# Optimization experiments

Measured on AMD Instinct MI355X. Metric: run time of the kernel, lower is better.

The kernel has to match this reference:

```python
import jax, jax.numpy as jnp
import numpy as np

NEG_SLOPE = 0.2
EPS = 1e-16


def gat_conv(x, edge_index, W, att_src, att_dst, bias, heads, out_ch, concat):
    """PyG-style GATConv (eval mode, add_self_loops=True)."""
    N = x.shape[0]
    h = (x @ W).reshape(N, heads, out_ch)              # [N,H,C]
    loop = jnp.arange(N, dtype=edge_index.dtype)
    src = jnp.concatenate([edge_index[0], loop])       # [E+N]
    dst = jnp.concatenate([edge_index[1], loop])
    a_src = jnp.sum(h * att_src, axis=-1)              # [N,H]
    a_dst = jnp.sum(h * att_dst, axis=-1)
    e = jax.nn.leaky_relu(a_src[src] + a_dst[dst], NEG_SLOPE)  # [E+N,H]
    # segment softmax over destination nodes
    m = jax.ops.segment_max(e, dst, num_segments=N)
    e = jnp.exp(e - m[dst])
    s = jax.ops.segment_sum(e, dst, num_segments=N)
    alpha = e / (s[dst] + EPS)                         # [E+N,H]
    msg = h[src] * alpha[..., None]                    # [E+N,H,C]
    out = jax.ops.segment_sum(msg, dst, num_segments=N)  # [N,H,C]
    out = out.reshape(N, heads * out_ch) if concat else out.mean(axis=1)
    return out + bias


def setup_inputs() -> dict:
    key = jax.random.key(0)
    ks = jax.random.split(key, 11)
    N, F, E = 100000, 128, 1600000
    H1, C1 = 4, 16
    H2, C2 = 1, 16
    return {
        "x": jax.random.normal(ks[0], (N, F), dtype=jnp.float32),
        "edge_index": jax.random.randint(ks[1], (2, E), 0, N, dtype=jnp.int64) if jax.config.jax_enable_x64 else jax.random.randint(ks[1], (2, E), 0, N).astype(jnp.int32),
        "W1": jax.random.normal(ks[2], (F, H1 * C1), dtype=jnp.float32) * 0.1,
        "att_src1": jax.random.normal(ks[3], (H1, C1), dtype=jnp.float32) * 0.1,
        "att_dst1": jax.random.normal(ks[4], (H1, C1), dtype=jnp.float32) * 0.1,
        "bias1": jax.random.normal(ks[5], (H1 * C1,), dtype=jnp.float32) * 0.1,
        "W2": jax.random.normal(ks[6], (H1 * C1, H2 * C2), dtype=jnp.float32) * 0.1,
        "att_src2": jax.random.normal(ks[7], (H2, C2), dtype=jnp.float32) * 0.1,
        "att_dst2": jax.random.normal(ks[8], (H2, C2), dtype=jnp.float32) * 0.1,
        "bias2": jax.random.normal(ks[9], (C2,), dtype=jnp.float32) * 0.1,
    }


def reference(x, edge_index, W1, att_src1, att_dst1, bias1, W2, att_src2, att_dst2, bias2):
    # dropout is identity in eval mode
    h = gat_conv(x, edge_index, W1, att_src1, att_dst1, bias1, heads=4, out_ch=16, concat=True)
    h = jax.nn.elu(h)
    h = gat_conv(h, edge_index, W2, att_src2, att_dst2, bias2, heads=1, out_ch=16, concat=False)
    return jax.nn.log_softmax(h, axis=1)
```

## Files before the change

### kernel.cpp

```cpp
#include <hip/hip_runtime.h>
#include <hip/hip_fp16.h>
#include <hip/hip_bf16.h>
#include <math.h>


#define LRELU(v) ((v) > 0.f ? (v) : 0.2f * (v))
#define CAP 128
#define BSH 8
#define BCAP 5120
#define CHK 2048

typedef __attribute__((ext_vector_type(8))) short short8;
typedef __attribute__((ext_vector_type(4))) float float4v;

static __device__ __forceinline__ short f2bf(float f) {
    __hip_bfloat16 b = __float2bfloat16(f);
    return *reinterpret_cast<short*>(&b);
}

__global__ __launch_bounds__(256) void k_scatter(const int* __restrict__ ei, int* __restrict__ cursor,
                                                 int* __restrict__ stage, int E, int NBK) {
    __shared__ int sval[CHK];
    __shared__ int gaddr[CHK];
    __shared__ int sdst[CHK];
    __shared__ int hist[512];
    __shared__ int lbase[512];
    __shared__ int cnt2[512];
    __shared__ int gdelta[512];
    __shared__ int sA[512];
    int tid = threadIdx.x;
    int e0 = blockIdx.x * CHK;
    int nedge = E - e0; if (nedge > CHK) nedge = CHK;

    for (int i = tid; i < 512; i += 256) { hist[i] = 0; cnt2[i] = 0; }
    __syncthreads();
    for (int j = tid; j < nedge; j += 256) {
        int d = ei[E + e0 + j];
        sdst[j] = d;
        atomicAdd(&hist[d >> BSH], 1);
    }
    __syncthreads();
    sA[tid] = hist[tid]; sA[tid + 256] = hist[tid + 256];
    __syncthreads();
    for (int off = 1; off < 512; off <<= 1) {
        int r0 = sA[tid] + ((tid >= off) ? sA[tid - off] : 0);
        int r1 = sA[tid + 256] + ((tid + 256 >= off) ? sA[tid + 256 - off] : 0);
        __syncthreads();
        sA[tid] = r0; sA[tid + 256] = r1;
        __syncthreads();
    }
    for (int i = tid; i < 512; i += 256) lbase[i] = sA[i] - hist[i];
    __syncthreads();
    for (int b = tid; b < NBK; b += 256) {
        int c = hist[b];
        if (c > 0) {
            int rel = atomicAdd(&cursor[b], c);
            gdelta[b] = b * BCAP + rel - lbase[b];
        }
    }
    __syncthreads();
    for (int j = tid; j < nedge; j += 256) {
        int s = ei[e0 + j];
        int d = sdst[j];
        int b = d >> BSH;
        int r = atomicAdd(&cnt2[b], 1);
        int slot = lbase[b] + r;
        sval[slot]  = s | ((d & ((1 << BSH) - 1)) << 17);
        gaddr[slot] = gdelta[b] + slot;
    }
    __syncthreads();
    for (int s = tid; s < nedge; s += 256) stage[gaddr[s]] = sval[s];
}

__global__ __launch_bounds__(256) void k_bucket_scan(const int* __restrict__ cursor,
                                                     int* __restrict__ gbase,
                                                     int* __restrict__ row_start,
                                                     int NBK, int E, int N) {
    __shared__ int sA[512];
    __shared__ int cnt[512];
    int tid = threadIdx.x;
    for (int i = tid; i < 512; i += 256)
        cnt[i] = (i < NBK) ? cursor[i] : 0;
    __syncthreads();
    sA[tid] = cnt[tid]; sA[tid + 256] = cnt[tid + 256];
    __syncthreads();
    for (int off = 1; off < 512; off <<= 1) {
        int r0 = sA[tid] + ((tid >= off) ? sA[tid - off] : 0);
        int r1 = sA[tid + 256] + ((tid + 256 >= off) ? sA[tid + 256 - off] : 0);
        __syncthreads();
        sA[tid] = r0; sA[tid + 256] = r1;
        __syncthreads();
    }
    for (int i = tid; i < 512; i += 256)
        if (i < NBK) gbase[i] = sA[i] - cnt[i];
    if (tid == 0) { gbase[NBK] = E; row_start[N] = E + N; }
}

__global__ __launch_bounds__(256) void k_build(const int* __restrict__ stage,
                                               const int* __restrict__ gbase,
                                               int* __restrict__ row_start,
                                               int* __restrict__ csr, int N) {
    __shared__ int cnt[256];
    __shared__ int lb[256];
    __shared__ int cur[256];
    __shared__ int sA[256];
    int b = blockIdx.x, tid = threadIdx.x;
    int nodes0 = b << BSH;
    int nnodes = N - nodes0; if (nnodes > 256) nnodes = 256;
    int ebase = gbase[b];
    int ecnt = gbase[b + 1] - ebase;
    const int* sbk = stage + b * BCAP;
    cnt[tid] = (tid < nnodes) ? 1 : 0;
    __syncthreads();
    for (int e = tid; e < ecnt; e += 256) {
        int l = (sbk[e] >> 17) & 255;
        atomicAdd(&cnt[l], 1);
    }
    __syncthreads();
    int myc = cnt[tid];
    sA[tid] = myc;
    __syncthreads();
    for (int off = 1; off < 256; off <<= 1) {
        int r = sA[tid] + ((tid >= off) ? sA[tid - off] : 0);
        __syncthreads();
        sA[tid] = r;
        __syncthreads();
    }
    int gb = ebase + nodes0;
    lb[tid] = sA[tid] - myc;
    cur[tid] = 1;
    __syncthreads();
    if (tid < nnodes) {
        row_start[nodes0 + tid] = gb + lb[tid];
        csr[gb + lb[tid]] = nodes0 + tid;
    }
    __syncthreads();
    for (int e = tid; e < ecnt; e += 256) {
        int v = sbk[e];
        int l = (v >> 17) & 255;
        int src = v & 0x1FFFF;
        int r = atomicAdd(&cur[l], 1);
        csr[gb + lb[l] + r] = src;
    }
}

__global__ __launch_bounds__(128) void k_watt(const float* __restrict__ W1,
                                              const float* __restrict__ att_src,
                                              const float* __restrict__ att_dst,
                                              float* __restrict__ Wc) {
    int k = threadIdx.x;
    #pragma unroll
    for (int h = 0; h < 4; h++) {
        float s = 0.f, d = 0.f;
        #pragma unroll
        for (int c = 0; c < 16; c++) {
            float w = W1[k * 64 + h * 16 + c];
            s += w * att_src[h * 16 + c];
            d += w * att_dst[h * 16 + c];
        }
        Wc[h * 128 + k] = s;
        Wc[(4 + h) * 128 + k] = d;
    }
    #pragma unroll
    for (int col = 8; col < 16; col++) Wc[col * 128 + k] = 0.f;
}

__global__ __launch_bounds__(256) void k_gemm1(const float* __restrict__ x,
                                               const float* __restrict__ W1,
                                               const float* __restrict__ Wc,
                                               __half* __restrict__ h1, float* __restrict__ a_src,
                                               float* __restrict__ a_dst, int N) {
    __shared__ short wt[80 * 136];
    int tid = threadIdx.x;
    for (int i = tid; i < 128 * 64; i += 256) {
        int k = i >> 6, c = i & 63;
        wt[c * 136 + k] = f2bf(W1[i]);
    }
    for (int i = tid; i < 16 * 128; i += 256) {
        int col = i >> 7, k = i & 127;
        wt[(64 + col) * 136 + k] = f2bf(Wc[i]);
    }
    __syncthreads();
    int wave = tid >> 6, lane = tid & 63;
    int m = lane & 15, q = lane >> 4;
    int nbase = blockIdx.x * 64 + wave * 16;
    int anode = nbase + m;
    bool rowok = anode < N;
    const float* xrow = x + (size_t)(rowok ? anode : 0) * 128 + q * 8;

    float4v acc[5];
    #pragma unroll
    for (int ct = 0; ct < 5; ct++)
        #pragma unroll
        for (int r = 0; r < 4; r++) acc[ct][r] = 0.f;

    #pragma unroll
    for (int kc = 0; kc < 4; kc++) {
        float4 u0 = make_float4(0.f, 0.f, 0.f, 0.f), u1 = u0;
        if (rowok) {
            u0 = *(const float4*)(xrow + kc * 32);
            u1 = *(const float4*)(xrow + kc * 32 + 4);
        }
        short8 af;
        af[0] = f2bf(u0.x); af[1] = f2bf(u0.y); af[2] = f2bf(u0.z); af[3] = f2bf(u0.w);
        af[4] = f2bf(u1.x); af[5] = f2bf(u1.y); af[6] = f2bf(u1.z); af[7] = f2bf(u1.w);
        #pragma unroll
        for (int ct = 0; ct < 5; ct++) {
            short8 bf = *(const short8*)&wt[(ct * 16 + m) * 136 + kc * 32 + q * 8];
            acc[ct] = __builtin_amdgcn_mfma_f32_16x16x32_bf16(af, bf, acc[ct], 0, 0, 0);
        }
    }
    #pragma unroll
    for (int ct = 0; ct < 4; ct++) {
        #pragma unroll
        for (int r = 0; r < 4; r++) {
            int n = nbase + q * 4 + r;
            if (n < N) h1[(size_t)n * 64 + ct * 16 + m] = __float2half(acc[ct][r]);
        }
    }
    #pragma unroll
    for (int r = 0; r < 4; r++) {
        int n = nbase + q * 4 + r;
        if (n < N) {
            float v = acc[4][r];
            if (m < 4) a_src[n * 4 + m] = v;
            else if (m < 8) a_dst[n * 4 + (m - 4)] = v;
        }
    }
}

__global__ __launch_bounds__(256) void k_agg1(const int* __restrict__ row_start,
                                              const int* __restrict__ csr_src,
                                              const float* __restrict__ a_src,
                                              const float* __restrict__ a_dst,
                                              const __half* __restrict__ h1,
                                              const float* __restrict__ bias,
                                              float* __restrict__ out1, int N) {
    __shared__ int   sidx[4][CAP];
    __shared__ float sval[4][CAP * 4];
    int wave = threadIdx.x >> 6, lane = threadIdx.x & 63;
    int node = blockIdx.x * 4 + wave;
    if (node >= N) return;
    int row = row_start[node];
    int deg = row_start[node + 1] - row;
    float4 ad = ((const float4*)a_dst)[node];
    float s0 = 0.f, s1 = 0.f, s2 = 0.f, s3 = 0.f;
    for (int j = lane; j < deg; j += 64) {
        int s = csr_src[row + j];
        float4 as = ((const float4*)a_src)[s];
        float e0 = __expf(LRELU(as.x + ad.x));
        float e1 = __expf(LRELU(as.y + ad.y));
        float e2 = __expf(LRELU(as.z + ad.z));
        float e3 = __expf(LRELU(as.w + ad.w));
        if (j < CAP) {
            sidx[wave][j] = s;
            *(float4*)&sval[wave][j * 4] = make_float4(e0, e1, e2, e3);
        }
        s0 += e0; s1 += e1; s2 += e2; s3 += e3;
    }
    #pragma unroll
    for (int m = 1; m < 64; m <<= 1) {
        s0 += __shfl_xor(s0, m, 64);
        s1 += __shfl_xor(s1, m, 64);
        s2 += __shfl_xor(s2, m, 64);
        s3 += __shfl_xor(s3, m, 64);
    }
    int myh = lane >> 4;
    float ssv = myh == 0 ? s0 : myh == 1 ? s1 : myh == 2 ? s2 : s3;
    float adm = myh == 0 ? ad.x : myh == 1 ? ad.y : myh == 2 ? ad.z : ad.w;
    float iv = 1.f / (ssv + 1e-16f);
    float acc = 0.f, accB = 0.f;
    int dc = deg < CAP ? deg : CAP;
    int j = 0;
    for (; j + 8 <= dc; j += 8) {
        int t0 = sidx[wave][j + 0], t1 = sidx[wave][j + 1];
        int t2 = sidx[wave][j + 2], t3 = sidx[wave][j + 3];
        int t4 = sidx[wave][j + 4], t5 = sidx[wave][j + 5];
        int t6 = sidx[wave][j + 6], t7 = sidx[wave][j + 7];
        float e0 = sval[wave][(j + 0) * 4 + myh], e1 = sval[wave][(j + 1) * 4 + myh];
        float e2 = sval[wave][(j + 2) * 4 + myh], e3 = sval[wave][(j + 3) * 4 + myh];
        float e4 = sval[wave][(j + 4) * 4 + myh], e5 = sval[wave][(j + 5) * 4 + myh];
        float e6 = sval[wave][(j + 6) * 4 + myh], e7 = sval[wave][(j + 7) * 4 + myh];
        float g0 = __half2float(h1[(size_t)t0 * 64 + lane]);
        float g1 = __half2float(h1[(size_t)t1 * 64 + lane]);
        float g2 = __half2float(h1[(size_t)t2 * 64 + lane]);
        float g3 = __half2float(h1[(size_t)t3 * 64 + lane]);
        float g4 = __half2float(h1[(size_t)t4 * 64 + lane]);
        float g5 = __half2float(h1[(size_t)t5 * 64 + lane]);
        float g6 = __half2float(h1[(size_t)t6 * 64 + lane]);
        float g7 = __half2float(h1[(size_t)t7 * 64 + lane]);
        acc  += e0 * g0 + e2 * g2 + e4 * g4 + e6 * g6;
        accB += e1 * g1 + e3 * g3 + e5 * g5 + e7 * g7;
    }
    for (; j + 4 <= dc; j += 4) {
        int t0 = sidx[wave][j + 0], t1 = sidx[wave][j + 1];
        int t2 = sidx[wave][j + 2], t3 = sidx[wave][j + 3];
        float e0 = sval[wave][(j + 0) * 4 + myh], e1 = sval[wave][(j + 1) * 4 + myh];
        float e2 = sval[wave][(j + 2) * 4 + myh], e3 = sval[wave][(j + 3) * 4 + myh];
        float g0 = __half2float(h1[(size_t)t0 * 64 + lane]);
        float g1 = __half2float(h1[(size_t)t1 * 64 + lane]);
        float g2 = __half2float(h1[(size_t)t2 * 64 + lane]);
        float g3 = __half2float(h1[(size_t)t3 * 64 + lane]);
        acc  += e0 * g0 + e2 * g2;
        accB += e1 * g1 + e3 * g3;
    }
    for (; j < dc; j++)
        acc += sval[wave][j * 4 + myh] * __half2float(h1[(size_t)sidx[wave][j] * 64 + lane]);
    for (; j < deg; j++) {
        int s = csr_src[row + j];
        float e = __expf(LRELU(a_src[s * 4 + myh] + adm));
        acc += e * __half2float(h1[(size_t)s * 64 + lane]);
    }
    acc = (acc + accB) * iv;
    float o = acc + bias[lane];
    o = (o > 0.f) ? o : (__expf(o) - 1.f);
    out1[(size_t)node * 64 + lane] = o;
}

__global__ __launch_bounds__(256) void k_gemm2(const float* __restrict__ out1,
                                               const float* __restrict__ W2,
                                               const float* __restrict__ att_src,
                                               const float* __restrict__ att_dst,
                                               float* __restrict__ h2, float* __restrict__ a_src,
                                               float* __restrict__ a_dst, int N) {
    __shared__ float ws[64 * 16];
    __shared__ float xs[16 * 65];
    int tid = threadIdx.x;
    for (int i = tid; i < 64 * 16; i += 256) ws[i] = W2[i];
    int n0 = blockIdx.x * 16;
    for (int i = tid; i < 16 * 64; i += 256) {
        int r = i >> 6, c = i & 63;
        int n = n0 + r;
        xs[r * 65 + c] = (n < N) ? out1[(size_t)n * 64 + c] : 0.f;
    }
    __syncthreads();
    int nl = tid >> 4, c = tid & 15;
    int n = n0 + nl;
    float acc = 0.f;
    #pragma unroll
    for (int k = 0; k < 64; k++) acc += xs[nl * 65 + k] * ws[k * 16 + c];
    float asv = acc * att_src[c];
    float adv = acc * att_dst[c];
    #pragma unroll
    for (int m = 1; m < 16; m <<= 1) {
        asv += __shfl_xor(asv, m, 64);
        adv += __shfl_xor(adv, m, 64);
    }
    if (n < N) {
        h2[(size_t)n * 16 + c] = acc;
        if (c == 0) { a_src[n] = asv; a_dst[n] = adv; }
    }
}

#define CAP2 64
__global__ __launch_bounds__(256) void k_agg2(const int* __restrict__ row_start,
                                              const int* __restrict__ csr_src,
                                              const float* __restrict__ a_src,
                                              const float* __restrict__ a_dst,
                                              const float* __restrict__ h2,
                                              const float* __restrict__ bias,
                                              float* __restrict__ out, int N) {
    __shared__ int   sidx[4][2][CAP2];
    __shared__ float sval[4][2][CAP2];
    int wave = threadIdx.x >> 6, lane = threadIdx.x & 63;
    int half = lane >> 5, l32 = lane & 31;
    int node = blockIdx.x * 8 + wave * 2 + half;
    if (node >= N) return;
    int row = row_start[node];
    int deg = row_start[node + 1] - row;
    float ad = a_dst[node];
    float sh = 0.f;
    for (int j = l32; j < deg; j += 32) {
        int s = csr_src[row + j];
        float e = __expf(LRELU(a_src[s] + ad));
        if (j < CAP2) { sidx[wave][half][j] = s; sval[wave][half][j] = e; }
        sh += e;
    }
    #pragma unroll
    for (int m = 1; m < 32; m <<= 1) sh += __shfl_xor(sh, m, 64);
    float iv = 1.f / (sh + 1e-16f);
    int c = l32 & 15, sub = l32 >> 4;
    float acc = 0.f, acc2 = 0.f;
    int dc = deg < CAP2 ? deg : CAP2;
    int j = sub;
    for (; j + 2 < dc; j += 4) {
        int t0 = sidx[wave][half][j], t1 = sidx[wave][half][j + 2];
        float e0 = sval[wave][half][j], e1 = sval[wave][half][j + 2];
        float g0 = h2[(size_t)t0 * 16 + c], g1 = h2[(size_t)t1 * 16 + c];
        acc += e0 * g0; acc2 += e1 * g1;
    }
    for (; j < deg; j += 2) {
        int s; float e;
        if (j < dc) { s = sidx[wave][half][j]; e = sval[wave][half][j]; }
        else { s = csr_src[row + j]; e = __expf(LRELU(a_src[s] + ad)); }
        acc += e * h2[(size_t)s * 16 + c];
    }
    acc += acc2;
    acc += __shfl_xor(acc, 16, 64);
    float val = acc * iv + bias[c];
    float mx = val;
    #pragma unroll
    for (int m = 1; m < 16; m <<= 1) mx = fmaxf(mx, __shfl_xor(mx, m, 64));
    float se = __expf(val - mx);
    #pragma unroll
    for (int m = 1; m < 16; m <<= 1) se += __shfl_xor(se, m, 64);
    float o = val - mx - __logf(se);
    if (sub == 0) out[(size_t)node * 16 + c] = o;
}

extern "C" void kernel_launch(void* const* d_in, const int* in_sizes, int n_in,
                              void* d_out, int out_size, void* d_ws, size_t ws_size,
                              hipStream_t stream) {
    const float* x        = (const float*)d_in[0];
    const int*   ei       = (const int*)d_in[1];
    const float* W1       = (const float*)d_in[2];
    const float* att_src1 = (const float*)d_in[3];
    const float* att_dst1 = (const float*)d_in[4];
    const float* bias1    = (const float*)d_in[5];
    const float* W2       = (const float*)d_in[6];
    const float* att_src2 = (const float*)d_in[7];
    const float* att_dst2 = (const float*)d_in[8];
    const float* bias2    = (const float*)d_in[9];
    float* out = (float*)d_out;

    const int N = in_sizes[0] / 128;
    const int E = in_sizes[1] / 2;
    const int NBK = (N + 255) >> BSH;

    char* p = (char*)d_ws;
    auto alloc = [&](size_t bytes) -> void* {
        void* r = (void*)p;
        p += (bytes + 255) & ~(size_t)255;
        return r;
    };
    __half* h1     = (__half*)alloc((size_t)N * 64 * 2);
    float* out1    = (float*)alloc((size_t)N * 64 * 4);
    float* h2      = (float*)alloc((size_t)N * 16 * 4);
    float* a_src1  = (float*)alloc((size_t)N * 4 * 4);
    float* a_dst1  = (float*)alloc((size_t)N * 4 * 4);
    float* a_src2  = (float*)alloc((size_t)N * 4);
    float* a_dst2  = (float*)alloc((size_t)N * 4);
    float* Wc      = (float*)alloc(16 * 128 * 4);
    int*   row_st  = (int*)alloc((size_t)(N + 1) * 4);
    int*   csr     = (int*)alloc((size_t)(E + N) * 4);
    int*   stage   = (int*)alloc((size_t)NBK * BCAP * 4);
    int*   cursor  = (int*)alloc((size_t)NBK * 4);
    int*   gbase   = (int*)alloc((size_t)(NBK + 1) * 4);
    (void)ws_size; (void)n_in; (void)out_size;

    hipMemsetAsync(cursor, 0, (size_t)NBK * 4, stream);
    k_watt<<<1, 128, 0, stream>>>(W1, att_src1, att_dst1, Wc);
    k_scatter<<<(E + CHK - 1) / CHK, 256, 0, stream>>>(ei, cursor, stage, E, NBK);
    k_bucket_scan<<<1, 256, 0, stream>>>(cursor, gbase, row_st, NBK, E, N);
    k_build<<<NBK, 256, 0, stream>>>(stage, gbase, row_st, csr, N);
    k_gemm1<<<(N + 63) / 64, 256, 0, stream>>>(x, W1, Wc, h1, a_src1, a_dst1, N);
    k_agg1<<<(N + 3) / 4, 256, 0, stream>>>(row_st, csr, a_src1, a_dst1, h1, bias1, out1, N);
    k_gemm2<<<(N + 15) / 16, 256, 0, stream>>>(out1, W2, att_src2, att_dst2, h2, a_src2, a_dst2, N);
    k_agg2<<<(N + 7) / 8, 256, 0, stream>>>(row_st, csr, a_src2, a_dst2, h2, bias2, out, N);
}
```

Baseline: 282.0 us.

## Pack two nodes per wave in layer-1 aggregation and store h2 as fp16

```diff
diff --git a/kernel.cpp b/kernel.cpp
--- a/kernel.cpp
+++ b/kernel.cpp
@@ -5,10 +5,11 @@
 
 
 #define LRELU(v) ((v) > 0.f ? (v) : 0.2f * (v))
-#define CAP 128
 #define BSH 8
 #define BCAP 5120
 #define CHK 2048
+#define CAP1 64
+#define CAP2 64
 
 typedef __attribute__((ext_vector_type(8))) short short8;
 typedef __attribute__((ext_vector_type(4))) float float4v;
@@ -236,92 +237,91 @@
                                               const __half* __restrict__ h1,
                                               const float* __restrict__ bias,
                                               float* __restrict__ out1, int N) {
-    __shared__ int   sidx[4][CAP];
-    __shared__ float sval[4][CAP * 4];
+    __shared__ int   sidx[4][2][CAP1];
+    __shared__ float sval[4][2][CAP1 * 4];
     int wave = threadIdx.x >> 6, lane = threadIdx.x & 63;
-    int node = blockIdx.x * 4 + wave;
+    int half = lane >> 5, l32 = lane & 31;
+    int node = blockIdx.x * 8 + wave * 2 + half;
     if (node >= N) return;
     int row = row_start[node];
     int deg = row_start[node + 1] - row;
     float4 ad = ((const float4*)a_dst)[node];
     float s0 = 0.f, s1 = 0.f, s2 = 0.f, s3 = 0.f;
-    for (int j = lane; j < deg; j += 64) {
+    for (int j = l32; j < deg; j += 32) {
         int s = csr_src[row + j];
         float4 as = ((const float4*)a_src)[s];
         float e0 = __expf(LRELU(as.x + ad.x));
         float e1 = __expf(LRELU(as.y + ad.y));
         float e2 = __expf(LRELU(as.z + ad.z));
         float e3 = __expf(LRELU(as.w + ad.w));
-        if (j < CAP) {
-            sidx[wave][j] = s;
-            *(float4*)&sval[wave][j * 4] = make_float4(e0, e1, e2, e3);
+        if (j < CAP1) {
+            sidx[wave][half][j] = s;
+            *(float4*)&sval[wave][half][j * 4] = make_float4(e0, e1, e2, e3);
         }
         s0 += e0; s1 += e1; s2 += e2; s3 += e3;
     }
     #pragma unroll
-    for (int m = 1; m < 64; m <<= 1) {
+    for (int m = 1; m < 32; m <<= 1) {
         s0 += __shfl_xor(s0, m, 64);
         s1 += __shfl_xor(s1, m, 64);
         s2 += __shfl_xor(s2, m, 64);
         s3 += __shfl_xor(s3, m, 64);
     }
-    int myh = lane >> 4;
+    int myh = l32 >> 3;
     float ssv = myh == 0 ? s0 : myh == 1 ? s1 : myh == 2 ? s2 : s3;
     float adm = myh == 0 ? ad.x : myh == 1 ? ad.y : myh == 2 ? ad.z : ad.w;
     float iv = 1.f / (ssv + 1e-16f);
-    float acc = 0.f, accB = 0.f;
-    int dc = deg < CAP ? deg : CAP;
+    float ax = 0.f, ay = 0.f, bx = 0.f, by = 0.f;
+    int dc = deg < CAP1 ? deg : CAP1;
     int j = 0;
     for (; j + 8 <= dc; j += 8) {
-        int t0 = sidx[wave][j + 0], t1 = sidx[wave][j + 1];
-        int t2 = sidx[wave][j + 2], t3 = sidx[wave][j + 3];
-        int t4 = sidx[wave][j + 4], t5 = sidx[wave][j + 5];
-        int t6 = sidx[wave][j + 6], t7 = sidx[wave][j + 7];
-        float e0 = sval[wave][(j + 0) * 4 + myh], e1 = sval[wave][(j + 1) * 4 + myh];
-        float e2 = sval[wave][(j + 2) * 4 + myh], e3 = sval[wave][(j + 3) * 4 + myh];
-        float e4 = sval[wave][(j + 4) * 4 + myh], e5 = sval[wave][(j + 5) * 4 + myh];
-        float e6 = sval[wave][(j + 6) * 4 + myh], e7 = sval[wave][(j + 7) * 4 + myh];
-        float g0 = __half2float(h1[(size_t)t0 * 64 + lane]);
-        float g1 = __half2float(h1[(size_t)t1 * 64 + lane]);
-        float g2 = __half2float(h1[(size_t)t2 * 64 + lane]);
-        float g3 = __half2float(h1[(size_t)t3 * 64 + lane]);
-        float g4 = __half2float(h1[(size_t)t4 * 64 + lane]);
-        float g5 = __half2float(h1[(size_t)t5 * 64 + lane]);
-        float g6 = __half2float(h1[(size_t)t6 * 64 + lane]);
-        float g7 = __half2float(h1[(size_t)t7 * 64 + lane]);
-        acc  += e0 * g0 + e2 * g2 + e4 * g4 + e6 * g6;
-        accB += e1 * g1 + e3 * g3 + e5 * g5 + e7 * g7;
-    }
-    for (; j + 4 <= dc; j += 4) {
-        int t0 = sidx[wave][j + 0], t1 = sidx[wave][j + 1];
-        int t2 = sidx[wave][j + 2], t3 = sidx[wave][j + 3];
-        float e0 = sval[wave][(j + 0) * 4 + myh], e1 = sval[wave][(j + 1) * 4 + myh];
-        float e2 = sval[wave][(j + 2) * 4 + myh], e3 = sval[wave][(j + 3) * 4 + myh];
-        float g0 = __half2float(h1[(size_t)t0 * 64 + lane]);
-        float g1 = __half2float(h1[(size_t)t1 * 64 + lane]);
-        float g2 = __half2float(h1[(size_t)t2 * 64 + lane]);
-        float g3 = __half2float(h1[(size_t)t3 * 64 + lane]);
-        acc  += e0 * g0 + e2 * g2;
-        accB += e1 * g1 + e3 * g3;
-    }
-    for (; j < dc; j++)
-        acc += sval[wave][j * 4 + myh] * __half2float(h1[(size_t)sidx[wave][j] * 64 + lane]);
+        int t0 = sidx[wave][half][j + 0], t1 = sidx[wave][half][j + 1];
+        int t2 = sidx[wave][half][j + 2], t3 = sidx[wave][half][j + 3];
+        int t4 = sidx[wave][half][j + 4], t5 = sidx[wave][half][j + 5];
+        int t6 = sidx[wave][half][j + 6], t7 = sidx[wave][half][j + 7];
+        float e0 = sval[wave][half][(j + 0) * 4 + myh], e1 = sval[wave][half][(j + 1) * 4 + myh];
+        float e2 = sval[wave][half][(j + 2) * 4 + myh], e3 = sval[wave][half][(j + 3) * 4 + myh];
+        float e4 = sval[wave][half][(j + 4) * 4 + myh], e5 = sval[wave][half][(j + 5) * 4 + myh];
+        float e6 = sval[wave][half][(j + 6) * 4 + myh], e7 = sval[wave][half][(j + 7) * 4 + myh];
+        float2 g0 = __half22float2(*(const __half2*)&h1[(size_t)t0 * 64 + l32 * 2]);
+        float2 g1 = __half22float2(*(const __half2*)&h1[(size_t)t1 * 64 + l32 * 2]);
+        float2 g2 = __half22float2(*(const __half2*)&h1[(size_t)t2 * 64 + l32 * 2]);
+        float2 g3 = __half22float2(*(const __half2*)&h1[(size_t)t3 * 64 + l32 * 2]);
+        float2 g4 = __half22float2(*(const __half2*)&h1[(size_t)t4 * 64 + l32 * 2]);
+        float2 g5 = __half22float2(*(const __half2*)&h1[(size_t)t5 * 64 + l32 * 2]);
+        float2 g6 = __half22float2(*(const __half2*)&h1[(size_t)t6 * 64 + l32 * 2]);
+        float2 g7 = __half22float2(*(const __half2*)&h1[(size_t)t7 * 64 + l32 * 2]);
+        ax += e0 * g0.x + e2 * g2.x + e4 * g4.x + e6 * g6.x;
+        ay += e0 * g0.y + e2 * g2.y + e4 * g4.y + e6 * g6.y;
+        bx += e1 * g1.x + e3 * g3.x + e5 * g5.x + e7 * g7.x;
+        by += e1 * g1.y + e3 * g3.y + e5 * g5.y + e7 * g7.y;
+    }
+    for (; j < dc; j++) {
+        int t = sidx[wave][half][j];
+        float e = sval[wave][half][j * 4 + myh];
+        float2 g = __half22float2(*(const __half2*)&h1[(size_t)t * 64 + l32 * 2]);
+        ax += e * g.x; ay += e * g.y;
+    }
     for (; j < deg; j++) {
         int s = csr_src[row + j];
         float e = __expf(LRELU(a_src[s * 4 + myh] + adm));
-        acc += e * __half2float(h1[(size_t)s * 64 + lane]);
-    }
-    acc = (acc + accB) * iv;
-    float o = acc + bias[lane];
-    o = (o > 0.f) ? o : (__expf(o) - 1.f);
-    out1[(size_t)node * 64 + lane] = o;
+        float2 g = __half22float2(*(const __half2*)&h1[(size_t)s * 64 + l32 * 2]);
+        ax += e * g.x; ay += e * g.y;
+    }
+    ax += bx; ay += by;
+    float2 bb = ((const float2*)bias)[l32];
+    float ox = ax * iv + bb.x;
+    float oy = ay * iv + bb.y;
+    ox = (ox > 0.f) ? ox : (__expf(ox) - 1.f);
+    oy = (oy > 0.f) ? oy : (__expf(oy) - 1.f);
+    ((float2*)out1)[(size_t)node * 32 + l32] = make_float2(ox, oy);
 }
 
 __global__ __launch_bounds__(256) void k_gemm2(const float* __restrict__ out1,
                                                const float* __restrict__ W2,
                                                const float* __restrict__ att_src,
                                                const float* __restrict__ att_dst,
-                                               float* __restrict__ h2, float* __restrict__ a_src,
+                                               __half* __restrict__ h2, float* __restrict__ a_src,
                                                float* __restrict__ a_dst, int N) {
     __shared__ float ws[64 * 16];
     __shared__ float xs[16 * 65];
@@ -347,17 +347,16 @@
         adv += __shfl_xor(adv, m, 64);
     }
     if (n < N) {
-        h2[(size_t)n * 16 + c] = acc;
+        h2[(size_t)n * 16 + c] = __float2half(acc);
         if (c == 0) { a_src[n] = asv; a_dst[n] = adv; }
     }
 }
 
-#define CAP2 64
 __global__ __launch_bounds__(256) void k_agg2(const int* __restrict__ row_start,
                                               const int* __restrict__ csr_src,
                                               const float* __restrict__ a_src,
                                               const float* __restrict__ a_dst,
-                                              const float* __restrict__ h2,
+                                              const __half* __restrict__ h2,
                                               const float* __restrict__ bias,
                                               float* __restrict__ out, int N) {
     __shared__ int   sidx[4][2][CAP2];
@@ -379,33 +378,43 @@
     #pragma unroll
     for (int m = 1; m < 32; m <<= 1) sh += __shfl_xor(sh, m, 64);
     float iv = 1.f / (sh + 1e-16f);
-    int c = l32 & 15, sub = l32 >> 4;
-    float acc = 0.f, acc2 = 0.f;
+    int cg = l32 & 7, eg = l32 >> 3;
+    float ax = 0.f, ay = 0.f, bx = 0.f, by = 0.f;
     int dc = deg < CAP2 ? deg : CAP2;
-    int j = sub;
-    for (; j + 2 < dc; j += 4) {
-        int t0 = sidx[wave][half][j], t1 = sidx[wave][half][j + 2];
-        float e0 = sval[wave][half][j], e1 = sval[wave][half][j + 2];
-        float g0 = h2[(size_t)t0 * 16 + c], g1 = h2[(size_t)t1 * 16 + c];
-        acc += e0 * g0; acc2 += e1 * g1;
-    }
-    for (; j < deg; j += 2) {
+    int j = eg;
+    for (; j + 4 < dc; j += 8) {
+        int t0 = sidx[wave][half][j], t1 = sidx[wave][half][j + 4];
+        float e0 = sval[wave][half][j], e1 = sval[wave][half][j + 4];
+        float2 g0 = __half22float2(*(const __half2*)&h2[(size_t)t0 * 16 + cg * 2]);
+        float2 g1 = __half22float2(*(const __half2*)&h2[(size_t)t1 * 16 + cg * 2]);
+        ax += e0 * g0.x; ay += e0 * g0.y;
+        bx += e1 * g1.x; by += e1 * g1.y;
+    }
+    for (; j < deg; j += 4) {
         int s; float e;
         if (j < dc) { s = sidx[wave][half][j]; e = sval[wave][half][j]; }
         else { s = csr_src[row + j]; e = __expf(LRELU(a_src[s] + ad)); }
-        acc += e * h2[(size_t)s * 16 + c];
-    }
-    acc += acc2;
-    acc += __shfl_xor(acc, 16, 64);
-    float val = acc * iv + bias[c];
-    float mx = val;
-    #pragma unroll
-    for (int m = 1; m < 16; m <<= 1) mx = fmaxf(mx, __shfl_xor(mx, m, 64));
-    float se = __expf(val - mx);
-    #pragma unroll
-    for (int m = 1; m < 16; m <<= 1) se += __shfl_xor(se, m, 64);
-    float o = val - mx - __logf(se);
-    if (sub == 0) out[(size_t)node * 16 + c] = o;
+        float2 g = __half22float2(*(const __half2*)&h2[(size_t)s * 16 + cg * 2]);
+        ax += e * g.x; ay += e * g.y;
+    }
+    ax += bx; ay += by;
+    #pragma unroll
+    for (int m = 8; m < 32; m <<= 1) {
+        ax += __shfl_xor(ax, m, 64);
+        ay += __shfl_xor(ay, m, 64);
+    }
+    float2 bb = ((const float2*)bias)[cg];
+    float vx = ax * iv + bb.x;
+    float vy = ay * iv + bb.y;
+    float mx = fmaxf(vx, vy);
+    #pragma unroll
+    for (int m = 1; m < 8; m <<= 1) mx = fmaxf(mx, __shfl_xor(mx, m, 64));
+    float se = __expf(vx - mx) + __expf(vy - mx);
+    #pragma unroll
+    for (int m = 1; m < 8; m <<= 1) se += __shfl_xor(se, m, 64);
+    float ls = mx + __logf(se);
+    if (eg == 0)
+        ((float2*)out)[(size_t)node * 8 + cg] = make_float2(vx - ls, vy - ls);
 }
 
 extern "C" void kernel_launch(void* const* d_in, const int* in_sizes, int n_in,
@@ -435,7 +444,7 @@
     };
     __half* h1     = (__half*)alloc((size_t)N * 64 * 2);
     float* out1    = (float*)alloc((size_t)N * 64 * 4);
-    float* h2      = (float*)alloc((size_t)N * 16 * 4);
+    __half* h2     = (__half*)alloc((size_t)N * 16 * 2);
     float* a_src1  = (float*)alloc((size_t)N * 4 * 4);
     float* a_dst1  = (float*)alloc((size_t)N * 4 * 4);
     float* a_src2  = (float*)alloc((size_t)N * 4);
@@ -454,7 +463,7 @@
     k_bucket_scan<<<1, 256, 0, stream>>>(cursor, gbase, row_st, NBK, E, N);
     k_build<<<NBK, 256, 0, stream>>>(stage, gbase, row_st, csr, N);
     k_gemm1<<<(N + 63) / 64, 256, 0, stream>>>(x, W1, Wc, h1, a_src1, a_dst1, N);
-    k_agg1<<<(N + 3) / 4, 256, 0, stream>>>(row_st, csr, a_src1, a_dst1, h1, bias1, out1, N);
+    k_agg1<<<(N + 7) / 8, 256, 0, stream>>>(row_st, csr, a_src1, a_dst1, h1, bias1, out1, N);
     k_gemm2<<<(N + 15) / 16, 256, 0, stream>>>(out1, W2, att_src2, att_dst2, h2, a_src2, a_dst2, N);
     k_agg2<<<(N + 7) / 8, 256, 0, stream>>>(row_st, csr, a_src2, a_dst2, h2, bias2, out, N);
 }
```

Result: faster. 263.2 us (-6.6%).
